# Kernel tuning notes

Measured on AMD Instinct MI355X. Metric: run time of the kernel, lower is better.

The kernel has to match this reference:

```python
import jax, jax.numpy as jnp
import numpy as np

D_MODEL, N_HEADS = 768, 12
D_K = D_MODEL // N_HEADS
NEG = -1e9


def setup_inputs() -> dict:
    key = jax.random.key(0)
    ks = jax.random.split(key, 12)
    B, S, D = 2, 4096, D_MODEL
    s = 1.0 / np.sqrt(D)
    inp = {
        'query': jax.random.normal(ks[0], (B, S, D), jnp.float32),
        'key': jax.random.normal(ks[1], (B, S, D), jnp.float32),
        'value': jax.random.normal(ks[2], (B, S, D), jnp.float32),
        'mask': jnp.ones((B, S), jnp.int32),
        'Wq': jax.random.normal(ks[3], (D, D), jnp.float32) * s,
        'bq': jnp.zeros((D,), jnp.float32),
        'Wk': jax.random.normal(ks[4], (D, D), jnp.float32) * s,
        'bk': jnp.zeros((D,), jnp.float32),
        'Wv': jax.random.normal(ks[5], (D, D), jnp.float32) * s,
        'bv': jnp.zeros((D,), jnp.float32),
        'Wo': jax.random.normal(ks[6], (D, D), jnp.float32) * s,
        'bo': jnp.zeros((D,), jnp.float32),
    }
    return inp


def reference(query, key, value, mask, Wq, bq, Wk, bk, Wv, bv, Wo, bo):
    B, Sq, D = query.shape
    Sk = key.shape[1]
    # torch Linear: x @ W.T + b; weights stored [out, in]
    def proj(x, W, b, S):
        return (x @ W.T + b).reshape(B, S, N_HEADS, D_K).transpose(0, 2, 1, 3)
    Q = proj(query, Wq, bq, Sq)   # [B,H,Sq,Dk]
    K = proj(key, Wk, bk, Sk)
    V = proj(value, Wv, bv, Sk)
    scores = jnp.einsum('bhqd,bhkd->bhqk', Q, K) / jnp.sqrt(jnp.float32(D_K))
    # padding mask on keys: [B,1,1,Sk]
    scores = jnp.where(mask[:, None, None, :] == 0, NEG, scores)
    # causal mask (triu, diagonal=1)
    causal = jnp.triu(jnp.ones((Sq, Sk), bool), k=1)
    scores = jnp.where(causal[None, None], NEG, scores)
    attn = jax.nn.softmax(scores, axis=-1)
    out = jnp.einsum('bhqk,bhkd->bhqd', attn, V)
    out = out.transpose(0, 2, 1, 3).reshape(B, Sq, D)
    return out @ Wo.T + bo
```

## Files before the change

### kernel.cpp

```cpp
#include <hip/hip_runtime.h>
#include <hip/hip_bf16.h>

#define D_MODEL 768
#define N_HEADS 12
#define D_K     64
#define NEG_INF (-1e9f)
#define SCALE_Q 0.1803368801111154f
#define W_ELEMS (D_MODEL * D_MODEL)

typedef __attribute__((ext_vector_type(8))) short          bf16x8;
typedef __attribute__((ext_vector_type(4))) float          floatx4;
typedef __attribute__((ext_vector_type(4))) unsigned short ushortx4;
typedef __attribute__((ext_vector_type(2))) unsigned int   uintx2;
typedef __attribute__((ext_vector_type(4))) unsigned int   uintx4;

static __device__ __forceinline__ unsigned short f2bf(float f) {
    unsigned u = __builtin_bit_cast(unsigned, f);
    u += 0x7FFFu + ((u >> 16) & 1u);
    return (unsigned short)(u >> 16);
}

static __device__ __forceinline__ void gload_lds16(const void* g, void* l) {
    __builtin_amdgcn_global_load_lds(
        (const __attribute__((address_space(1))) void*)g,
        (__attribute__((address_space(3))) void*)l, 16, 0, 0);
}

__global__ __launch_bounds__(256) void convert_w4(
    const float* __restrict__ W0, const float* __restrict__ W1,
    const float* __restrict__ W2, const float* __restrict__ W3,
    unsigned short* __restrict__ out)
{
    const float* src[4] = {W0, W1, W2, W3};
    const float* W = src[blockIdx.y];
    unsigned short* o = out + (size_t)blockIdx.y * W_ELEMS;
    const int i = (blockIdx.x * 256 + threadIdx.x) * 4;
    float4 v = *(const float4*)(W + i);
    ushortx4 h = { f2bf(v.x), f2bf(v.y), f2bf(v.z), f2bf(v.w) };
    *(ushortx4*)(o + i) = h;
}

__global__ __launch_bounds__(256) void convert_a3(
    const float* __restrict__ A0, const float* __restrict__ A1,
    const float* __restrict__ A2,
    unsigned short* __restrict__ O0, unsigned short* __restrict__ O1,
    unsigned short* __restrict__ O2)
{
    const int z = blockIdx.y;
    const float* A = (z == 0) ? A0 : (z == 1) ? A1 : A2;
    unsigned short* O = (z == 0) ? O0 : (z == 1) ? O1 : O2;
    const int i = (blockIdx.x * 256 + threadIdx.x) * 4;
    float4 v = *(const float4*)(A + i);
    ushortx4 h = { f2bf(v.x), f2bf(v.y), f2bf(v.z), f2bf(v.w) };
    *(ushortx4*)(O + i) = h;
}

__global__ __launch_bounds__(256) void gemm128(
    const unsigned short* __restrict__ A0, const unsigned short* __restrict__ A1,
    const unsigned short* __restrict__ A2,
    const unsigned short* __restrict__ W0, const unsigned short* __restrict__ W1,
    const unsigned short* __restrict__ W2,
    const float* __restrict__ b0, const float* __restrict__ b1,
    const float* __restrict__ b2,
    void* __restrict__ C0, void* __restrict__ C1, void* __restrict__ C2,
    int S)
{
    __shared__ __align__(16) unsigned short As[128 * 32];
    __shared__ __align__(16) unsigned short Bs[128 * 32];

    const int z = blockIdx.z;
    const unsigned short* A = (z == 0) ? A0 : (z == 1) ? A1 : A2;
    const unsigned short* W = (z == 0) ? W0 : (z == 1) ? W1 : W2;
    const float* bias       = (z == 0) ? b0 : (z == 1) ? b1 : b2;
    void* C                 = (z == 0) ? C0 : (z == 1) ? C1 : C2;
    const float scale = (z == 0) ? SCALE_Q : 1.0f;
    const int mode = (z == 2) ? 3 : 1;

    const int tid  = threadIdx.x;
    const int wave = tid >> 6;
    const int lane = tid & 63;
    const int quad = lane >> 4;
    const int l16  = lane & 15;
    const int m0 = blockIdx.x * 128;
    const int n0 = blockIdx.y * 128;
    const int wm = (wave & 1) * 64;
    const int wn = (wave >> 1) * 64;
    const int sr = lane >> 2;
    const int sc = (lane & 3) << 3;

    const floatx4 zero4 = {0.f, 0.f, 0.f, 0.f};
    floatx4 acc[4][4];
    #pragma unroll
    for (int i = 0; i < 4; ++i)
        #pragma unroll
        for (int j = 0; j < 4; ++j) acc[i][j] = zero4;

    for (int k0 = 0; k0 < D_MODEL; k0 += 32) {
        #pragma unroll
        for (int c = 0; c < 2; ++c) {
            const int row = wave * 32 + c * 16;
            gload_lds16(A + (size_t)(m0 + row + sr) * D_MODEL + k0 + sc,
                        As + row * 32);
            gload_lds16(W + (size_t)(n0 + row + sr) * D_MODEL + k0 + sc,
                        Bs + row * 32);
        }
        __syncthreads();

        bf16x8 af[4], bfr[4];
        #pragma unroll
        for (int i = 0; i < 4; ++i)
            af[i] = *(const bf16x8*)(As + (wm + i * 16 + l16) * 32 + quad * 8);
        #pragma unroll
        for (int j = 0; j < 4; ++j)
            bfr[j] = *(const bf16x8*)(Bs + (wn + j * 16 + l16) * 32 + quad * 8);
        #pragma unroll
        for (int i = 0; i < 4; ++i)
            #pragma unroll
            for (int j = 0; j < 4; ++j)
                acc[i][j] = __builtin_amdgcn_mfma_f32_16x16x32_bf16(
                    bfr[j], af[i], acc[i][j], 0, 0, 0);
        __syncthreads();
    }

    #pragma unroll
    for (int i = 0; i < 4; ++i) {
        const int m = m0 + wm + i * 16 + l16;
        #pragma unroll
        for (int j = 0; j < 4; ++j) {
            const int nb = n0 + wn + j * 16 + quad * 4;
            const float4 bv = *(const float4*)(bias + nb);
            float v0 = (acc[i][j][0] + bv.x) * scale;
            float v1 = (acc[i][j][1] + bv.y) * scale;
            float v2 = (acc[i][j][2] + bv.z) * scale;
            float v3 = (acc[i][j][3] + bv.w) * scale;
            if (mode == 1) {
                ushortx4 o = {f2bf(v0), f2bf(v1), f2bf(v2), f2bf(v3)};
                *(ushortx4*)((unsigned short*)C + (size_t)m * D_MODEL + nb) = o;
            } else {
                const int bb = m / S, s = m - bb * S;
                const int hh = nb >> 6, d = nb & 63;
                unsigned short* base = (unsigned short*)C +
                    ((size_t)(bb * N_HEADS + hh) * D_K + d) * S + s;
                base[0]         = f2bf(v0);
                base[(size_t)S]     = f2bf(v1);
                base[(size_t)S * 2] = f2bf(v2);
                base[(size_t)S * 3] = f2bf(v3);
            }
        }
    }
}

__global__ __launch_bounds__(256) void gemm64o(
    const unsigned short* __restrict__ A,
    const unsigned short* __restrict__ W,
    const float* __restrict__ bias,
    float* __restrict__ C)
{
    __shared__ __align__(16) unsigned short As[64 * 32];
    __shared__ __align__(16) unsigned short Bs[128 * 32];

    const int tid  = threadIdx.x;
    const int wave = tid >> 6;
    const int lane = tid & 63;
    const int quad = lane >> 4;
    const int l16  = lane & 15;
    const int m0 = blockIdx.x * 64;
    const int n0 = blockIdx.y * 128;
    const int wn = wave * 32;
    const int sr = lane >> 2;
    const int sc = (lane & 3) << 3;

    const floatx4 zero4 = {0.f, 0.f, 0.f, 0.f};
    floatx4 acc[4][2];
    #pragma unroll
    for (int i = 0; i < 4; ++i)
        #pragma unroll
        for (int j = 0; j < 2; ++j) acc[i][j] = zero4;

    for (int k0 = 0; k0 < D_MODEL; k0 += 32) {
        if (wave < 2) {
            const int g0 = wave * 32;
            gload_lds16(A + (size_t)(m0 + g0 + sr) * D_MODEL + k0 + sc,
                        As + g0 * 32);
            gload_lds16(A + (size_t)(m0 + g0 + 16 + sr) * D_MODEL + k0 + sc,
                        As + (g0 + 16) * 32);
            const int bg = 96 + wave * 16;
            gload_lds16(W + (size_t)(n0 + bg + sr) * D_MODEL + k0 + sc,
                        Bs + bg * 32);
        } else {
            const int bg = (wave - 2) * 48;
            #pragma unroll
            for (int c = 0; c < 3; ++c)
                gload_lds16(W + (size_t)(n0 + bg + c * 16 + sr) * D_MODEL + k0 + sc,
                            Bs + (bg + c * 16) * 32);
        }
        __syncthreads();

        bf16x8 af[4], bfr[2];
        #pragma unroll
        for (int i = 0; i < 4; ++i)
            af[i] = *(const bf16x8*)(As + (i * 16 + l16) * 32 + quad * 8);
        #pragma unroll
        for (int j = 0; j < 2; ++j)
            bfr[j] = *(const bf16x8*)(Bs + (wn + j * 16 + l16) * 32 + quad * 8);
        #pragma unroll
        for (int i = 0; i < 4; ++i)
            #pragma unroll
            for (int j = 0; j < 2; ++j)
                acc[i][j] = __builtin_amdgcn_mfma_f32_16x16x32_bf16(
                    bfr[j], af[i], acc[i][j], 0, 0, 0);
        __syncthreads();
    }

    #pragma unroll
    for (int i = 0; i < 4; ++i) {
        const int m = m0 + i * 16 + l16;
        #pragma unroll
        for (int j = 0; j < 2; ++j) {
            const int nb = n0 + wn + j * 16 + quad * 4;
            const float4 bv = *(const float4*)(bias + nb);
            float4 o = {acc[i][j][0] + bv.x, acc[i][j][1] + bv.y,
                        acc[i][j][2] + bv.z, acc[i][j][3] + bv.w};
            *(float4*)(C + (size_t)m * D_MODEL + nb) = o;
        }
    }
}

__global__ __launch_bounds__(256) void flash_attn(
    const unsigned short* __restrict__ Qp,
    const unsigned short* __restrict__ Kp,
    const unsigned short* __restrict__ VpT,
    const int* __restrict__ mask,
    unsigned short* __restrict__ O,
    int S)
{
    __shared__ __align__(16) unsigned short Ks [128 * 64];
    __shared__ __align__(16) unsigned short Vts[64 * 128];
    __shared__ __align__(16) float mskf[128];

    const int L  = blockIdx.x;
    const int bh = L % 24;
    const int p  = L / 24;
    const int h  = bh % 12;
    const int b  = bh / 12;
    const int nqt = S >> 6;
    const int tid  = threadIdx.x;
    const int wave = tid >> 6;
    const int lane = tid & 63;
    const int quad = lane >> 4;
    const int l16  = lane & 15;
    const int sx   = (l16 & 7) << 3;

    const unsigned short* Kbase = Kp  + (size_t)(b * S) * D_MODEL + h * D_K;
    const unsigned short* Vbase = VpT + (size_t)(b * N_HEADS + h) * D_K * S;
    const int* mbase = mask + b * S;

    const int kgrow = wave * 32 + (lane >> 3);
    const int kgcol = ((lane & 7) ^ (lane >> 3)) << 3;
    const int vgrow = wave * 16 + (lane >> 4);
    const int vgc_e = ((lane & 15) ^ (lane >> 4)) << 3;
    const int vgc_o = ((lane & 15) ^ (4 + (lane >> 4))) << 3;

    const floatx4 zero4 = {0.f, 0.f, 0.f, 0.f};
    const short one_bf = (short)0x3F80;
    const bf16x8 ones = {one_bf, one_bf, one_bf, one_bf,
                         one_bf, one_bf, one_bf, one_bf};

    #pragma unroll
    for (int sel = 0; sel < 2; ++sel) {
        const int qt = sel ? (nqt - 1 - p) : p;
        const int q0 = qt * 64;
        const int qbase = q0 + wave * 16;
        const int qabs = qbase + l16;

        const size_t rowQ = (size_t)(b * S + qbase + l16) * D_MODEL + h * D_K;
        const bf16x8 qf0 = *(const bf16x8*)(Qp + rowQ + quad * 8);
        const bf16x8 qf1 = *(const bf16x8*)(Qp + rowQ + 32 + quad * 8);

        floatx4 acc2[4];
        floatx4 acc_l = zero4;
        #pragma unroll
        for (int dt = 0; dt < 4; ++dt) acc2[dt] = zero4;

        const int ni = (qt >> 1) + 1;
        for (int kt = 0; kt < ni; ++kt) {
            const int k0 = kt * 128;
            #pragma unroll
            for (int c = 0; c < 4; ++c) {
                gload_lds16(
                    Kbase + (size_t)(k0 + kgrow + c * 8) * D_MODEL + kgcol,
                    (char*)Ks + (wave * 4 + c) * 1024);
                const int vg = (c & 1) ? vgc_o : vgc_e;
                gload_lds16(
                    Vbase + (size_t)(vgrow + c * 4) * S + k0 + vg,
                    (char*)Vts + (wave * 4 + c) * 1024);
            }
            if (tid < 128)
                mskf[tid] = (mbase[k0 + tid] == 0) ? NEG_INF : 0.f;
            __syncthreads();

            floatx4 s[8];
            #pragma unroll
            for (int nt = 0; nt < 8; ++nt) {
                floatx4 c = *(const floatx4*)(mskf + nt * 16 + quad * 4);
                const unsigned short* kro = Ks + (nt * 16 + l16) * 64;
                bf16x8 kf0 = *(const bf16x8*)(kro + ((quad * 8) ^ sx));
                bf16x8 kf1 = *(const bf16x8*)(kro + ((32 + quad * 8) ^ sx));
                c = __builtin_amdgcn_mfma_f32_16x16x32_bf16(kf0, qf0, c, 0, 0, 0);
                c = __builtin_amdgcn_mfma_f32_16x16x32_bf16(kf1, qf1, c, 0, 0, 0);
                s[nt] = c;
            }

            if (kt == ni - 1) {
                #pragma unroll
                for (int nt = 0; nt < 8; ++nt) {
                    const int kb = k0 + nt * 16 + quad * 4;
                    #pragma unroll
                    for (int r = 0; r < 4; ++r)
                        if (kb + r > qabs) s[nt][r] = NEG_INF;
                }
            }

            unsigned pk0[8], pk1[8];
            #pragma unroll
            for (int nt = 0; nt < 8; ++nt) {
                const float e0 = __builtin_exp2f(s[nt][0]);
                const float e1 = __builtin_exp2f(s[nt][1]);
                const float e2 = __builtin_exp2f(s[nt][2]);
                const float e3 = __builtin_exp2f(s[nt][3]);
                pk0[nt] = __builtin_amdgcn_perm(__builtin_bit_cast(unsigned, e1),
                                                __builtin_bit_cast(unsigned, e0), 0x07060302u);
                pk1[nt] = __builtin_amdgcn_perm(__builtin_bit_cast(unsigned, e3),
                                                __builtin_bit_cast(unsigned, e2), 0x07060302u);
            }

            #pragma unroll
            for (int kh = 0; kh < 4; ++kh) {
                uintx2 a32 = __builtin_amdgcn_permlane32_swap(
                    pk0[2 * kh], pk0[2 * kh + 1], false, false);
                uintx2 b32 = __builtin_amdgcn_permlane32_swap(
                    pk1[2 * kh], pk1[2 * kh + 1], false, false);
                uintx2 a16 = __builtin_amdgcn_permlane16_swap(
                    a32[0], a32[1], false, false);
                uintx2 b16 = __builtin_amdgcn_permlane16_swap(
                    b32[0], b32[1], false, false);
                const uintx4 pw = {a16[0], b16[0], a16[1], b16[1]};
                const bf16x8 pf = __builtin_bit_cast(bf16x8, pw);
                #pragma unroll
                for (int dt = 0; dt < 4; ++dt) {
                    const unsigned short* vro = Vts + (dt * 16 + l16) * 128;
                    bf16x8 vf = *(const bf16x8*)(vro + ((kh * 32 + quad * 8) ^ sx));
                    acc2[dt] = __builtin_amdgcn_mfma_f32_16x16x32_bf16(pf, vf, acc2[dt], 0, 0, 0);
                }
                acc_l = __builtin_amdgcn_mfma_f32_16x16x32_bf16(pf, ones, acc_l, 0, 0, 0);
            }
            __syncthreads();
        }

        #pragma unroll
        for (int r = 0; r < 4; ++r) {
            const float inv = 1.f / acc_l[r];
            const int gq = qbase + quad * 4 + r;
            const size_t base = (size_t)(b * S + gq) * D_MODEL + h * D_K;
            #pragma unroll
            for (int dt = 0; dt < 4; ++dt)
                O[base + dt * 16 + l16] = f2bf(acc2[dt][r] * inv);
        }
        __syncthreads();
    }
}

extern "C" void kernel_launch(void* const* d_in, const int* in_sizes, int n_in,
                              void* d_out, int out_size, void* d_ws, size_t ws_size,
                              hipStream_t stream) {
    const float* query = (const float*)d_in[0];
    const float* key   = (const float*)d_in[1];
    const float* value = (const float*)d_in[2];
    const int*   mask  = (const int*)d_in[3];
    const float* Wq = (const float*)d_in[4];
    const float* bq = (const float*)d_in[5];
    const float* Wk = (const float*)d_in[6];
    const float* bk = (const float*)d_in[7];
    const float* Wv = (const float*)d_in[8];
    const float* bv = (const float*)d_in[9];
    const float* Wo = (const float*)d_in[10];
    const float* bo = (const float*)d_in[11];

    const int B  = 2;
    const int BS = in_sizes[3];
    const int S  = BS / B;
    const int M  = BS;

    unsigned short* Qp  = (unsigned short*)d_ws;
    unsigned short* Kp  = Qp  + (size_t)M * D_MODEL;
    unsigned short* VpT = Kp  + (size_t)M * D_MODEL;
    unsigned short* Obf = VpT + (size_t)M * D_MODEL;
    unsigned short* Wbf = Obf + (size_t)M * D_MODEL;
    unsigned short* Wqb = Wbf;
    unsigned short* Wkb = Wbf + (size_t)W_ELEMS;
    unsigned short* Wvb = Wbf + (size_t)W_ELEMS * 2;
    unsigned short* Wob = Wbf + (size_t)W_ELEMS * 3;
    unsigned short* ka = (unsigned short*)d_out;
    unsigned short* va = ka + (size_t)M * D_MODEL;

    dim3 blk(256);
    convert_w4<<<dim3(W_ELEMS / 1024, 4), blk, 0, stream>>>(Wq, Wk, Wv, Wo, Wbf);
    convert_a3<<<dim3((M * D_MODEL) / 1024, 3), blk, 0, stream>>>(
        query, key, value, Obf, ka, va);

    gemm128<<<dim3(M / 128, D_MODEL / 128, 3), blk, 0, stream>>>(
        Obf, ka, va, Wqb, Wkb, Wvb, bq, bk, bv, Qp, Kp, VpT, S);

    flash_attn<<<768, blk, 0, stream>>>(Qp, Kp, VpT, mask, Obf, S);

    gemm64o<<<dim3(M / 64, D_MODEL / 128), blk, 0, stream>>>(
        Obf, Wob, bo, (float*)d_out);
}
```

Baseline: 305.2 us.

## Split attention waves across query pairs and key halves with LDS reduction

Reorganizes the attention kernel so each wave handles two 16-row query groups over half of the 128-key tile, instead of one query group over all keys. Each K and V fragment read from LDS is then reused for two query groups, cutting LDS read traffic per MFMA, at the cost of a cross-wave reduction through LDS after the key loop. It also switches to hardware exp2 and reciprocal intrinsics, which may lose a little precision.

```diff
diff --git a/kernel.cpp b/kernel.cpp
--- a/kernel.cpp
+++ b/kernel.cpp
@@ -18,6 +18,22 @@
     unsigned u = __builtin_bit_cast(unsigned, f);
     u += 0x7FFFu + ((u >> 16) & 1u);
     return (unsigned short)(u >> 16);
+}
+
+static __device__ __forceinline__ float exp2_hw(float x) {
+#if __has_builtin(__builtin_amdgcn_exp2f)
+    return __builtin_amdgcn_exp2f(x);
+#else
+    return __builtin_exp2f(x);
+#endif
+}
+
+static __device__ __forceinline__ float rcp_hw(float x) {
+#if __has_builtin(__builtin_amdgcn_rcpf)
+    return __builtin_amdgcn_rcpf(x);
+#else
+    return 1.f / x;
+#endif
 }
 
 static __device__ __forceinline__ void gload_lds16(const void* g, void* l) {
@@ -250,6 +266,8 @@
     const int quad = lane >> 4;
     const int l16  = lane & 15;
     const int sx   = (l16 & 7) << 3;
+    const int qh   = wave & 1;
+    const int kh2  = wave >> 1;
 
     const unsigned short* Kbase = Kp  + (size_t)(b * S) * D_MODEL + h * D_K;
     const unsigned short* Vbase = VpT + (size_t)(b * N_HEADS + h) * D_K * S;
@@ -270,17 +288,24 @@
     for (int sel = 0; sel < 2; ++sel) {
         const int qt = sel ? (nqt - 1 - p) : p;
         const int q0 = qt * 64;
-        const int qbase = q0 + wave * 16;
-        const int qabs = qbase + l16;
-
-        const size_t rowQ = (size_t)(b * S + qbase + l16) * D_MODEL + h * D_K;
-        const bf16x8 qf0 = *(const bf16x8*)(Qp + rowQ + quad * 8);
-        const bf16x8 qf1 = *(const bf16x8*)(Qp + rowQ + 32 + quad * 8);
-
-        floatx4 acc2[4];
-        floatx4 acc_l = zero4;
-        #pragma unroll
-        for (int dt = 0; dt < 4; ++dt) acc2[dt] = zero4;
+
+        bf16x8 qf[2][2];
+        #pragma unroll
+        for (int qg = 0; qg < 2; ++qg) {
+            const size_t rowQ =
+                (size_t)(b * S + q0 + qh * 32 + qg * 16 + l16) * D_MODEL + h * D_K;
+            qf[qg][0] = *(const bf16x8*)(Qp + rowQ + quad * 8);
+            qf[qg][1] = *(const bf16x8*)(Qp + rowQ + 32 + quad * 8);
+        }
+
+        floatx4 acc2[2][4];
+        floatx4 accl[2];
+        #pragma unroll
+        for (int qg = 0; qg < 2; ++qg) {
+            accl[qg] = zero4;
+            #pragma unroll
+            for (int dt = 0; dt < 4; ++dt) acc2[qg][dt] = zero4;
+        }
 
         const int ni = (qt >> 1) + 1;
         for (int kt = 0; kt < ni; ++kt) {
@@ -299,72 +324,120 @@
                 mskf[tid] = (mbase[k0 + tid] == 0) ? NEG_INF : 0.f;
             __syncthreads();
 
-            floatx4 s[8];
-            #pragma unroll
-            for (int nt = 0; nt < 8; ++nt) {
-                floatx4 c = *(const floatx4*)(mskf + nt * 16 + quad * 4);
-                const unsigned short* kro = Ks + (nt * 16 + l16) * 64;
-                bf16x8 kf0 = *(const bf16x8*)(kro + ((quad * 8) ^ sx));
-                bf16x8 kf1 = *(const bf16x8*)(kro + ((32 + quad * 8) ^ sx));
-                c = __builtin_amdgcn_mfma_f32_16x16x32_bf16(kf0, qf0, c, 0, 0, 0);
-                c = __builtin_amdgcn_mfma_f32_16x16x32_bf16(kf1, qf1, c, 0, 0, 0);
-                s[nt] = c;
+            floatx4 s[4][2];
+            #pragma unroll
+            for (int nt = 0; nt < 4; ++nt) {
+                const int krow = kh2 * 64 + nt * 16 + l16;
+                const unsigned short* kro = Ks + krow * 64;
+                const bf16x8 kf0 = *(const bf16x8*)(kro + ((quad * 8) ^ sx));
+                const bf16x8 kf1 = *(const bf16x8*)(kro + ((32 + quad * 8) ^ sx));
+                const floatx4 cm =
+                    *(const floatx4*)(mskf + kh2 * 64 + nt * 16 + quad * 4);
+                #pragma unroll
+                for (int qg = 0; qg < 2; ++qg) {
+                    floatx4 c = cm;
+                    c = __builtin_amdgcn_mfma_f32_16x16x32_bf16(kf0, qf[qg][0], c, 0, 0, 0);
+                    c = __builtin_amdgcn_mfma_f32_16x16x32_bf16(kf1, qf[qg][1], c, 0, 0, 0);
+                    s[nt][qg] = c;
+                }
             }
 
             if (kt == ni - 1) {
                 #pragma unroll
-                for (int nt = 0; nt < 8; ++nt) {
-                    const int kb = k0 + nt * 16 + quad * 4;
+                for (int nt = 0; nt < 4; ++nt) {
+                    const int kb = k0 + kh2 * 64 + nt * 16 + quad * 4;
                     #pragma unroll
-                    for (int r = 0; r < 4; ++r)
-                        if (kb + r > qabs) s[nt][r] = NEG_INF;
-                }
-            }
-
-            unsigned pk0[8], pk1[8];
-            #pragma unroll
-            for (int nt = 0; nt < 8; ++nt) {
-                const float e0 = __builtin_exp2f(s[nt][0]);
-                const float e1 = __builtin_exp2f(s[nt][1]);
-                const float e2 = __builtin_exp2f(s[nt][2]);
-                const float e3 = __builtin_exp2f(s[nt][3]);
-                pk0[nt] = __builtin_amdgcn_perm(__builtin_bit_cast(unsigned, e1),
-                                                __builtin_bit_cast(unsigned, e0), 0x07060302u);
-                pk1[nt] = __builtin_amdgcn_perm(__builtin_bit_cast(unsigned, e3),
-                                                __builtin_bit_cast(unsigned, e2), 0x07060302u);
-            }
-
-            #pragma unroll
-            for (int kh = 0; kh < 4; ++kh) {
-                uintx2 a32 = __builtin_amdgcn_permlane32_swap(
-                    pk0[2 * kh], pk0[2 * kh + 1], false, false);
-                uintx2 b32 = __builtin_amdgcn_permlane32_swap(
-                    pk1[2 * kh], pk1[2 * kh + 1], false, false);
-                uintx2 a16 = __builtin_amdgcn_permlane16_swap(
-                    a32[0], a32[1], false, false);
-                uintx2 b16 = __builtin_amdgcn_permlane16_swap(
-                    b32[0], b32[1], false, false);
-                const uintx4 pw = {a16[0], b16[0], a16[1], b16[1]};
-                const bf16x8 pf = __builtin_bit_cast(bf16x8, pw);
+                    for (int qg = 0; qg < 2; ++qg) {
+                        const int qa = q0 + qh * 32 + qg * 16 + l16;
+                        #pragma unroll
+                        for (int r = 0; r < 4; ++r)
+                            if (kb + r > qa) s[nt][qg][r] = NEG_INF;
+                    }
+                }
+            }
+
+            unsigned pk0[4][2], pk1[4][2];
+            #pragma unroll
+            for (int nt = 0; nt < 4; ++nt)
+                #pragma unroll
+                for (int qg = 0; qg < 2; ++qg) {
+                    const float e0 = exp2_hw(s[nt][qg][0]);
+                    const float e1 = exp2_hw(s[nt][qg][1]);
+                    const float e2 = exp2_hw(s[nt][qg][2]);
+                    const float e3 = exp2_hw(s[nt][qg][3]);
+                    pk0[nt][qg] = __builtin_amdgcn_perm(
+                        __builtin_bit_cast(unsigned, e1),
+                        __builtin_bit_cast(unsigned, e0), 0x07060302u);
+                    pk1[nt][qg] = __builtin_amdgcn_perm(
+                        __builtin_bit_cast(unsigned, e3),
+                        __builtin_bit_cast(unsigned, e2), 0x07060302u);
+                }
+
+            #pragma unroll
+            for (int kh = 0; kh < 2; ++kh) {
+                bf16x8 pf[2];
+                #pragma unroll
+                for (int qg = 0; qg < 2; ++qg) {
+                    uintx2 a32 = __builtin_amdgcn_permlane32_swap(
+                        pk0[2 * kh][qg], pk0[2 * kh + 1][qg], false, false);
+                    uintx2 b32 = __builtin_amdgcn_permlane32_swap(
+                        pk1[2 * kh][qg], pk1[2 * kh + 1][qg], false, false);
+                    uintx2 a16 = __builtin_amdgcn_permlane16_swap(
+                        a32[0], a32[1], false, false);
+                    uintx2 b16 = __builtin_amdgcn_permlane16_swap(
+                        b32[0], b32[1], false, false);
+                    const uintx4 pw = {a16[0], b16[0], a16[1], b16[1]};
+                    pf[qg] = __builtin_bit_cast(bf16x8, pw);
+                }
                 #pragma unroll
                 for (int dt = 0; dt < 4; ++dt) {
-                    const unsigned short* vro = Vts + (dt * 16 + l16) * 128;
-                    bf16x8 vf = *(const bf16x8*)(vro + ((kh * 32 + quad * 8) ^ sx));
-                    acc2[dt] = __builtin_amdgcn_mfma_f32_16x16x32_bf16(pf, vf, acc2[dt], 0, 0, 0);
-                }
-                acc_l = __builtin_amdgcn_mfma_f32_16x16x32_bf16(pf, ones, acc_l, 0, 0, 0);
+                    const int vcol = kh2 * 64 + ((kh * 32 + quad * 8) ^ sx);
+                    const bf16x8 vf =
+                        *(const bf16x8*)(Vts + (dt * 16 + l16) * 128 + vcol);
+                    #pragma unroll
+                    for (int qg = 0; qg < 2; ++qg)
+                        acc2[qg][dt] = __builtin_amdgcn_mfma_f32_16x16x32_bf16(
+                            pf[qg], vf, acc2[qg][dt], 0, 0, 0);
+                }
+                #pragma unroll
+                for (int qg = 0; qg < 2; ++qg)
+                    accl[qg] = __builtin_amdgcn_mfma_f32_16x16x32_bf16(
+                        pf[qg], ones, accl[qg], 0, 0, 0);
             }
             __syncthreads();
         }
 
-        #pragma unroll
-        for (int r = 0; r < 4; ++r) {
-            const float inv = 1.f / acc_l[r];
-            const int gq = qbase + quad * 4 + r;
-            const size_t base = (size_t)(b * S + gq) * D_MODEL + h * D_K;
-            #pragma unroll
-            for (int dt = 0; dt < 4; ++dt)
-                O[base + dt * 16 + l16] = f2bf(acc2[dt][r] * inv);
+        float* Kf = (float*)Ks;
+        float* Vf = (float*)Vts;
+        if (kh2 == 1) {
+            #pragma unroll
+            for (int qg = 0; qg < 2; ++qg) {
+                #pragma unroll
+                for (int dt = 0; dt < 4; ++dt)
+                    *(floatx4*)(Kf + (qh * 8 + qg * 4 + dt) * 256 + lane * 4) =
+                        acc2[qg][dt];
+                *(floatx4*)(Vf + (qh * 2 + qg) * 256 + lane * 4) = accl[qg];
+            }
+        }
+        __syncthreads();
+        if (kh2 == 0) {
+            #pragma unroll
+            for (int qg = 0; qg < 2; ++qg) {
+                accl[qg] += *(const floatx4*)(Vf + (qh * 2 + qg) * 256 + lane * 4);
+                #pragma unroll
+                for (int dt = 0; dt < 4; ++dt)
+                    acc2[qg][dt] +=
+                        *(const floatx4*)(Kf + (qh * 8 + qg * 4 + dt) * 256 + lane * 4);
+                #pragma unroll
+                for (int r = 0; r < 4; ++r) {
+                    const float inv = rcp_hw(accl[qg][r]);
+                    const int gq = q0 + qh * 32 + qg * 16 + quad * 4 + r;
+                    const size_t base = (size_t)(b * S + gq) * D_MODEL + h * D_K;
+                    #pragma unroll
+                    for (int dt = 0; dt < 4; ++dt)
+                        O[base + dt * 16 + l16] = f2bf(acc2[qg][dt][r] * inv);
+                }
+            }
         }
         __syncthreads();
     }
```

Result: faster. 295.0 us (-3.3%).
